# Kernel optimization log

Measured on AMD Instinct MI355X. Metric: run time of the kernel, lower is better.

The kernel has to match this reference:

```python
import jax, jax.numpy as jnp
import numpy as np

DIM = 1024
N_HEADS = 16
HEAD_DIM = DIM // N_HEADS
SCALE = HEAD_DIM ** -0.5


def setup_inputs() -> dict:
    key = jax.random.key(0)
    kx, kq, kk, kv = jax.random.split(key, 4)
    x = jax.random.normal(kx, (2, 2048, DIM), dtype=jnp.float32)
    bv_q = jax.random.normal(kq, (N_HEADS, HEAD_DIM), dtype=jnp.float32) * 0.02
    bv_k = jax.random.normal(kk, (N_HEADS, HEAD_DIM), dtype=jnp.float32) * 0.02
    bv_v = jax.random.normal(kv, (N_HEADS, HEAD_DIM), dtype=jnp.float32) * 0.02
    return {"x": x, "bv_q": bv_q, "bv_k": bv_k, "bv_v": bv_v}


def reference(x, bv_q, bv_k, bv_v):
    B, T, D = x.shape
    H, HD = N_HEADS, HEAD_DIM
    x_h = x.reshape(B, T, H, HD)
    # sign-gated Q/K/V (sign of binding vectors; elementwise +/-1 gating)
    Q = x_h * jnp.sign(bv_q)  # [B,T,H,HD]
    K = x_h * jnp.sign(bv_k)
    V = x_h * jnp.sign(bv_v)
    # causal scores, sigmoid gating (no softmax)
    scores = jnp.einsum('bqhd,bkhd->bhqk', Q, K) * SCALE  # [B,H,T,T]
    causal = jnp.tril(jnp.ones((T, T), dtype=bool))
    attn = jnp.where(causal, jax.nn.sigmoid(scores * 4.0), 0.0)
    out = jnp.einsum('bhqk,bkhd->bqhd', attn, V)  # [B,T,H,HD]
    return out.reshape(B, T, D)
```

## Files before the change

### kernel.cpp

```cpp
#include <hip/hip_runtime.h>
#include <hip/hip_bf16.h>
#include <stdint.h>

#define DIM 1024
#define T_LEN 2048
#define NB 2
#define NH 16
#define HD 64
#define NQT 32

typedef float f32x4 __attribute__((ext_vector_type(4)));
typedef float f32x16 __attribute__((ext_vector_type(16)));
typedef __bf16 bf16x8 __attribute__((ext_vector_type(8)));
typedef __bf16 bf16x2 __attribute__((ext_vector_type(2)));
typedef unsigned int u32;
typedef unsigned int u32x4 __attribute__((ext_vector_type(4)));

__device__ __forceinline__ float sgnf(float v) {
    return (v > 0.f) ? 1.f : ((v < 0.f) ? -1.f : 0.f);
}

__device__ __forceinline__ float sigmoid_half(float v) {
    return __builtin_amdgcn_rcpf(1.f + __builtin_amdgcn_exp2f(-0.72134752f * v));
}

__device__ __forceinline__ u32 pack2(float p0, float p1) {
    bf16x2 t = {(__bf16)p0, (__bf16)p1};
    return __builtin_bit_cast(u32, t);
}

__device__ __forceinline__ void gload16(const __bf16* g, __bf16* l) {
    __builtin_amdgcn_global_load_lds(
        (__attribute__((address_space(1))) void*)g,
        (__attribute__((address_space(3))) void*)l,
        16, 0, 0);
}

__global__ __launch_bounds__(256) void prep_kernel(
    const float* __restrict__ x, __bf16* __restrict__ xb, __bf16* __restrict__ xt)
{
    __shared__ __align__(16) __bf16 tile[64][72];

    const int bid = blockIdx.x;
    const int h = bid & 15, tmp = bid >> 4, tt = tmp & 31, b = tmp >> 5;
    const int tid = threadIdx.x;
    const int r = tid >> 2, c0 = (tid & 3) * 16;

    const size_t rowbase = ((size_t)(b * T_LEN + tt * 64 + r)) * DIM + h * HD + c0;
    const float* xp = x + rowbase;

    __bf16 v[16];
    #pragma unroll
    for (int i = 0; i < 16; i += 4) {
        f32x4 f = *(const f32x4*)(xp + i);
        #pragma unroll
        for (int j = 0; j < 4; ++j) v[i + j] = (__bf16)f[j];
    }
    bf16x8 s0, s1;
    #pragma unroll
    for (int j = 0; j < 8; ++j) { s0[j] = v[j]; s1[j] = v[8 + j]; }
    *(bf16x8*)(xb + rowbase)     = s0;
    *(bf16x8*)(xb + rowbase + 8) = s1;
    *(bf16x8*)&tile[r][c0]     = s0;
    *(bf16x8*)&tile[r][c0 + 8] = s1;

    __syncthreads();

    const int d = tid >> 2, t0c = (tid & 3) * 16;
    __bf16 ov[16];
    #pragma unroll
    for (int i = 0; i < 16; ++i) ov[i] = tile[t0c + i][d];
    bf16x8 o0, o1;
    #pragma unroll
    for (int j = 0; j < 8; ++j) { o0[j] = ov[j]; o1[j] = ov[8 + j]; }
    const size_t obase = ((size_t)((b * NH + h) * HD + d)) * T_LEN + tt * 64 + t0c;
    *(bf16x8*)(xt + obase)     = o0;
    *(bf16x8*)(xt + obase + 8) = o1;
}

__global__ __launch_bounds__(256, 4) void mba_main(
    const __bf16* __restrict__ xb, const __bf16* __restrict__ xt,
    const float* __restrict__ bvq, const float* __restrict__ bvk,
    const float* __restrict__ bvv, float* __restrict__ out)
{
    __shared__ __align__(16) __bf16 Kb[3][64][64];
    __shared__ __align__(16) __bf16 Vb[2][64][64];

    const int bid = blockIdx.x;
    const int u = bid >> 5;
    const int jj = u >> 3, aa = u & 7;
    const int qt = 8 * jj + ((jj & 1) ? (7 - aa) : aa);
    const int bh = bid & 31;
    const int b = bh >> 4, h = bh & 15;
    const int q0 = qt * 64;

    const int tid = threadIdx.x;
    const int w = tid >> 6, l = tid & 63;
    const int c = l & 31, hi = l >> 5;
    const int qh = w & 1, sh = w >> 1;

    const size_t xb_bh = (size_t)b * T_LEN * DIM + h * HD;
    const size_t xt_bh = (size_t)((b * NH + h) * HD) * T_LEN;

    const int rr = l >> 3;
    const int sw = ((l & 7) ^ rr) << 3;

    auto STAGE_K = [&](int buf, int kvt) {
        const int kv0s = kvt * 64;
        #pragma unroll
        for (int pt = 0; pt < 2; ++pt) {
            const int r0 = w * 8 + pt * 32;
            gload16(xb + xb_bh + (size_t)(kv0s + r0 + rr) * DIM + sw, &Kb[buf][r0][0]);
        }
    };
    auto STAGE_V = [&](int buf, int kvt) {
        const int kv0s = kvt * 64;
        #pragma unroll
        for (int pt = 0; pt < 2; ++pt) {
            const int r0 = w * 8 + pt * 32;
            gload16(xt + xt_bh + (size_t)(r0 + rr) * T_LEN + kv0s + sw, &Vb[buf][r0][0]);
        }
    };

    STAGE_K(0, 0);
    STAGE_V(0, 0);
    if (qt >= 1) STAGE_K(1, 1);

    bf16x8 qa[4];
    {
        const float* bq = bvq + h * HD;
        const float* bk = bvk + h * HD;
        const int qrow = q0 + qh * 32 + c;
        #pragma unroll
        for (int m = 0; m < 4; ++m) {
            const int d0 = m * 16 + hi * 8;
            bf16x8 va = *(const bf16x8*)(xb + xb_bh + (size_t)qrow * DIM + d0);
            #pragma unroll
            for (int j = 0; j < 8; ++j) {
                float f = sgnf(bq[d0 + j]) * sgnf(bk[d0 + j]);
                qa[m][j] = (__bf16)((float)va[j] * f);
            }
        }
    }
    float sv[2];
    #pragma unroll
    for (int nd = 0; nd < 2; ++nd) sv[nd] = sgnf(bvv[h * HD + nd * 32 + c]);

    f32x16 o[2];
    #pragma unroll
    for (int nd = 0; nd < 2; ++nd)
        #pragma unroll
        for (int i = 0; i < 16; ++i) o[nd][i] = 0.f;

    int cur = 0;
    const int krow = sh * 32 + c;
    const int swz = (c & 7) << 4;

    for (int t = 0; t <= qt; ++t) {
        const bool last = (t == qt);
        if (last) { asm volatile("s_waitcnt vmcnt(0)" ::: "memory"); }
        else      { asm volatile("s_waitcnt vmcnt(2)" ::: "memory"); }
        __builtin_amdgcn_sched_barrier(0);
        __builtin_amdgcn_s_barrier();
        __builtin_amdgcn_sched_barrier(0);

        if (t + 1 <= qt) STAGE_V((t + 1) & 1, t + 1);
        __builtin_amdgcn_sched_barrier(0);
        if (t + 2 <= qt) {
            int stg = cur + 2; if (stg >= 3) stg -= 3;
            STAGE_K(stg, t + 2);
        }
        __builtin_amdgcn_sched_barrier(0);

        f32x16 ss;
        #pragma unroll
        for (int i = 0; i < 16; ++i) ss[i] = 0.f;
        #pragma unroll
        for (int m = 0; m < 4; ++m) {
            bf16x8 kf = *(const bf16x8*)((const char*)&Kb[cur][krow][0]
                          + ((m * 32 + hi * 16) ^ swz));
            ss = __builtin_amdgcn_mfma_f32_32x32x16_bf16(kf, qa[m], ss, 0, 0, 0);
        }

        u32 W[8];
        #pragma unroll
        for (int i = 0; i < 8; ++i) {
            const int r0 = 2 * i;
            const int sl = (r0 & 3) + 8 * (r0 >> 2) + 4 * hi;
            float p0 = sigmoid_half(ss[r0]);
            float p1 = sigmoid_half(ss[r0 + 1]);
            if (last) {
                const int sg = sh * 32 + sl;
                const int qg = qh * 32 + c;
                if (sg > qg)     p0 = 0.f;
                if (sg + 1 > qg) p1 = 0.f;
            }
            W[i] = pack2(p0, p1);
        }

        asm volatile("v_permlane32_swap_b32 %0, %1" : "+v"(W[0]), "+v"(W[2]));
        asm volatile("v_permlane32_swap_b32 %0, %1" : "+v"(W[1]), "+v"(W[3]));
        asm volatile("v_permlane32_swap_b32 %0, %1" : "+v"(W[4]), "+v"(W[6]));
        asm volatile("v_permlane32_swap_b32 %0, %1" : "+v"(W[5]), "+v"(W[7]));
        bf16x8 pa[2];
        pa[0] = __builtin_bit_cast(bf16x8, (u32x4){W[0], W[1], W[2], W[3]});
        pa[1] = __builtin_bit_cast(bf16x8, (u32x4){W[4], W[5], W[6], W[7]});

        #pragma unroll
        for (int m = 0; m < 2; ++m) {
            #pragma unroll
            for (int nd = 0; nd < 2; ++nd) {
                bf16x8 vf = *(const bf16x8*)((const char*)&Vb[t & 1][nd * 32 + c][0]
                              + ((sh * 64 + m * 32 + hi * 16) ^ swz));
                o[nd] = __builtin_amdgcn_mfma_f32_32x32x16_bf16(pa[m], vf, o[nd], 0, 0, 0);
            }
        }
        cur = (cur == 2) ? 0 : cur + 1;
    }

    __syncthreads();
    float (*osc)[64] = (float(*)[64]) & Kb[0][0][0];

    if (sh == 1) {
        #pragma unroll
        for (int r = 0; r < 16; ++r) {
            const int qloc = (r & 3) + 8 * (r >> 2) + 4 * hi;
            #pragma unroll
            for (int nd = 0; nd < 2; ++nd)
                osc[qh * 32 + qloc][nd * 32 + c] = o[nd][r];
        }
    }
    __syncthreads();
    if (sh == 0) {
        #pragma unroll
        for (int r = 0; r < 16; ++r) {
            const int qloc = (r & 3) + 8 * (r >> 2) + 4 * hi;
            const size_t row = (size_t)(b * T_LEN + q0 + qh * 32 + qloc) * DIM + h * HD;
            #pragma unroll
            for (int nd = 0; nd < 2; ++nd) {
                float val = (o[nd][r] + osc[qh * 32 + qloc][nd * 32 + c]) * sv[nd];
                out[row + nd * 32 + c] = val;
            }
        }
    }
}

__global__ __launch_bounds__(256) void mba_fallback(
    const float* __restrict__ x,
    const float* __restrict__ bvq,
    const float* __restrict__ bvk,
    const float* __restrict__ bvv,
    float* __restrict__ out)
{
    __shared__ __align__(16) __bf16 Kb[64][72];
    __shared__ __align__(16) __bf16 Vt[HD][72];
    __shared__ __align__(16) __bf16 Pb[4][16][72];

    const int bid = blockIdx.x;
    const int qt  = (NQT - 1) - (bid & (NQT - 1));
    const int bh  = bid >> 5;
    const int b   = bh >> 4;
    const int h   = bh & 15;

    const int tid = threadIdx.x;
    const int w   = tid >> 6;
    const int l   = tid & 63;
    const int lq  = l & 15;
    const int lh  = l >> 4;

    const int  q0    = qt * 64;
    const long xbase = ((long)b * T_LEN) * DIM + h * HD;

    bf16x8 qa[2];
    {
        const int   qrow = q0 + w * 16 + lq;
        const float* qp  = x + xbase + (long)qrow * DIM + lh * 8;
        const float* gp  = bvq + h * HD + lh * 8;
        #pragma unroll
        for (int ks = 0; ks < 2; ++ks)
            #pragma unroll
            for (int j = 0; j < 8; ++j)
                qa[ks][j] = (__bf16)(qp[ks * 32 + j] * sgnf(gp[ks * 32 + j]));
    }

    f32x4 o[4];
    #pragma unroll
    for (int n = 0; n < 4; ++n) o[n] = (f32x4){0.f, 0.f, 0.f, 0.f};

    const int r_st = tid >> 2;
    const int c0   = (tid & 3) * 16;
    const float* gk = bvk + h * HD + c0;
    const float* gv = bvv + h * HD + c0;

    for (int kvt = 0; kvt <= qt; ++kvt) {
        const int kv0 = kvt * 64;
        __syncthreads();
        {
            const float* kp = x + xbase + (long)(kv0 + r_st) * DIM + c0;
            __bf16 kb[16];
            #pragma unroll
            for (int i = 0; i < 16; ++i) kb[i] = (__bf16)(kp[i] * sgnf(gk[i]));
            *(bf16x8*)&Kb[r_st][c0]     = *(bf16x8*)&kb[0];
            *(bf16x8*)&Kb[r_st][c0 + 8] = *(bf16x8*)&kb[8];
            #pragma unroll
            for (int i = 0; i < 16; ++i)
                Vt[c0 + i][r_st] = (__bf16)(kp[i] * sgnf(gv[i]));
        }
        __syncthreads();

        f32x4 s[4];
        #pragma unroll
        for (int n = 0; n < 4; ++n) s[n] = (f32x4){0.f, 0.f, 0.f, 0.f};
        #pragma unroll
        for (int ks = 0; ks < 2; ++ks)
            #pragma unroll
            for (int n = 0; n < 4; ++n) {
                bf16x8 kf = *(const bf16x8*)&Kb[n * 16 + lq][ks * 32 + lh * 8];
                s[n] = __builtin_amdgcn_mfma_f32_16x16x32_bf16(qa[ks], kf, s[n], 0, 0, 0);
            }

        const bool diag = (kvt == qt);
        #pragma unroll
        for (int n = 0; n < 4; ++n)
            #pragma unroll
            for (int j = 0; j < 4; ++j) {
                float p = sigmoid_half(s[n][j]);
                if (diag && (n * 16 + lq) > (w * 16 + lh * 4 + j)) p = 0.f;
                Pb[w][lh * 4 + j][n * 16 + lq] = (__bf16)p;
            }

        #pragma unroll
        for (int ks = 0; ks < 2; ++ks) {
            bf16x8 pf = *(const bf16x8*)&Pb[w][lq][ks * 32 + lh * 8];
            #pragma unroll
            for (int n = 0; n < 4; ++n) {
                bf16x8 vf = *(const bf16x8*)&Vt[n * 16 + lq][ks * 32 + lh * 8];
                o[n] = __builtin_amdgcn_mfma_f32_16x16x32_bf16(pf, vf, o[n], 0, 0, 0);
            }
        }
    }

    float* op = out + ((long)b * T_LEN + q0 + w * 16) * DIM + h * HD;
    #pragma unroll
    for (int n = 0; n < 4; ++n)
        #pragma unroll
        for (int j = 0; j < 4; ++j)
            op[(long)(lh * 4 + j) * DIM + n * 16 + lq] = o[n][j];
}

extern "C" void kernel_launch(void* const* d_in, const int* in_sizes, int n_in,
                              void* d_out, int out_size, void* d_ws, size_t ws_size,
                              hipStream_t stream) {
    (void)in_sizes; (void)n_in; (void)out_size;
    const float* x   = (const float*)d_in[0];
    const float* bvq = (const float*)d_in[1];
    const float* bvk = (const float*)d_in[2];
    const float* bvv = (const float*)d_in[3];
    float* out = (float*)d_out;

    const size_t XB_BYTES = (size_t)NB * T_LEN * DIM * sizeof(__bf16);
    const size_t XT_BYTES = XB_BYTES;

    if (ws_size < XB_BYTES + XT_BYTES) {
        mba_fallback<<<NB * NH * NQT, 256, 0, stream>>>(x, bvq, bvk, bvv, out);
        return;
    }

    __bf16* xb = (__bf16*)d_ws;
    __bf16* xt = xb + (size_t)NB * T_LEN * DIM;

    prep_kernel<<<NB * NQT * NH, 256, 0, stream>>>(x, xb, xt);
    mba_main<<<NB * NH * NQT, 256, 0, stream>>>(xb, xt, bvq, bvk, bvv, out);
}
```

Baseline: 47.43 us.

## Fold V sign into prep, switch to double-buffered K/V with priority hints

Moves the sign(bv_v) gating into the transpose prep kernel, so the main kernel no longer multiplies the output by sv at the epilogue. Replaces the 3-stage K ring with 2-stage K/V double buffering that issues both loads one tile ahead and waits on vmcnt(0) every iteration, unrolling the loop by two so buffer indices are constant. Adds s_setprio around the MFMA blocks and a packed-vector form of the sigmoid. The change reduces LDS use but gives K loads less prefetch distance, which may expose more memory latency.

Result: slower. 54.10 us (+14.1%).

```diff
diff --git a/kernel.cpp b/kernel.cpp
--- a/kernel.cpp
+++ b/kernel.cpp
@@ -9,6 +9,7 @@
 #define HD 64
 #define NQT 32
 
+typedef float f32x2 __attribute__((ext_vector_type(2)));
 typedef float f32x4 __attribute__((ext_vector_type(4)));
 typedef float f32x16 __attribute__((ext_vector_type(16)));
 typedef __bf16 bf16x8 __attribute__((ext_vector_type(8)));
@@ -20,10 +21,6 @@
     return (v > 0.f) ? 1.f : ((v < 0.f) ? -1.f : 0.f);
 }
 
-__device__ __forceinline__ float sigmoid_half(float v) {
-    return __builtin_amdgcn_rcpf(1.f + __builtin_amdgcn_exp2f(-0.72134752f * v));
-}
-
 __device__ __forceinline__ u32 pack2(float p0, float p1) {
     bf16x2 t = {(__bf16)p0, (__bf16)p1};
     return __builtin_bit_cast(u32, t);
@@ -37,7 +34,8 @@
 }
 
 __global__ __launch_bounds__(256) void prep_kernel(
-    const float* __restrict__ x, __bf16* __restrict__ xb, __bf16* __restrict__ xt)
+    const float* __restrict__ x, const float* __restrict__ bvv,
+    __bf16* __restrict__ xb, __bf16* __restrict__ xt)
 {
     __shared__ __align__(16) __bf16 tile[64][72];
 
@@ -67,9 +65,10 @@
     __syncthreads();
 
     const int d = tid >> 2, t0c = (tid & 3) * 16;
+    const float g = sgnf(bvv[h * HD + d]);
     __bf16 ov[16];
     #pragma unroll
-    for (int i = 0; i < 16; ++i) ov[i] = tile[t0c + i][d];
+    for (int i = 0; i < 16; ++i) ov[i] = (__bf16)((float)tile[t0c + i][d] * g);
     bf16x8 o0, o1;
     #pragma unroll
     for (int j = 0; j < 8; ++j) { o0[j] = ov[j]; o1[j] = ov[8 + j]; }
@@ -81,9 +80,9 @@
 __global__ __launch_bounds__(256, 4) void mba_main(
     const __bf16* __restrict__ xb, const __bf16* __restrict__ xt,
     const float* __restrict__ bvq, const float* __restrict__ bvk,
-    const float* __restrict__ bvv, float* __restrict__ out)
+    float* __restrict__ out)
 {
-    __shared__ __align__(16) __bf16 Kb[3][64][64];
+    __shared__ __align__(16) __bf16 Kb[2][64][64];
     __shared__ __align__(16) __bf16 Vb[2][64][64];
 
     const int bid = blockIdx.x;
@@ -124,7 +123,6 @@
 
     STAGE_K(0, 0);
     STAGE_V(0, 0);
-    if (qt >= 1) STAGE_K(1, 1);
 
     bf16x8 qa[4];
     {
@@ -142,9 +140,6 @@
             }
         }
     }
-    float sv[2];
-    #pragma unroll
-    for (int nd = 0; nd < 2; ++nd) sv[nd] = sgnf(bvv[h * HD + nd * 32 + c]);
 
     f32x16 o[2];
     #pragma unroll
@@ -152,44 +147,46 @@
         #pragma unroll
         for (int i = 0; i < 16; ++i) o[nd][i] = 0.f;
 
-    int cur = 0;
     const int krow = sh * 32 + c;
     const int swz = (c & 7) << 4;
 
-    for (int t = 0; t <= qt; ++t) {
-        const bool last = (t == qt);
-        if (last) { asm volatile("s_waitcnt vmcnt(0)" ::: "memory"); }
-        else      { asm volatile("s_waitcnt vmcnt(2)" ::: "memory"); }
+    auto bodyfn = [&](int t, int pb) {
+        const bool diag = (t == qt);
+        asm volatile("s_waitcnt vmcnt(0)" ::: "memory");
         __builtin_amdgcn_sched_barrier(0);
         __builtin_amdgcn_s_barrier();
         __builtin_amdgcn_sched_barrier(0);
 
-        if (t + 1 <= qt) STAGE_V((t + 1) & 1, t + 1);
+        if (t + 1 <= qt) {
+            STAGE_V(pb ^ 1, t + 1);
+            STAGE_K(pb ^ 1, t + 1);
+        }
         __builtin_amdgcn_sched_barrier(0);
-        if (t + 2 <= qt) {
-            int stg = cur + 2; if (stg >= 3) stg -= 3;
-            STAGE_K(stg, t + 2);
-        }
-        __builtin_amdgcn_sched_barrier(0);
 
         f32x16 ss;
         #pragma unroll
         for (int i = 0; i < 16; ++i) ss[i] = 0.f;
+        __builtin_amdgcn_s_setprio(1);
         #pragma unroll
         for (int m = 0; m < 4; ++m) {
-            bf16x8 kf = *(const bf16x8*)((const char*)&Kb[cur][krow][0]
+            bf16x8 kf = *(const bf16x8*)((const char*)&Kb[pb][krow][0]
                           + ((m * 32 + hi * 16) ^ swz));
             ss = __builtin_amdgcn_mfma_f32_32x32x16_bf16(kf, qa[m], ss, 0, 0, 0);
         }
+        __builtin_amdgcn_s_setprio(0);
 
         u32 W[8];
         #pragma unroll
         for (int i = 0; i < 8; ++i) {
             const int r0 = 2 * i;
             const int sl = (r0 & 3) + 8 * (r0 >> 2) + 4 * hi;
-            float p0 = sigmoid_half(ss[r0]);
-            float p1 = sigmoid_half(ss[r0 + 1]);
-            if (last) {
+            f32x2 z = {ss[r0], ss[r0 + 1]};
+            z = z * (-0.72134752f);
+            f32x2 e = {__builtin_amdgcn_exp2f(z.x), __builtin_amdgcn_exp2f(z.y)};
+            e = e + 1.0f;
+            float p0 = __builtin_amdgcn_rcpf(e.x);
+            float p1 = __builtin_amdgcn_rcpf(e.y);
+            if (diag) {
                 const int sg = sh * 32 + sl;
                 const int qg = qh * 32 + c;
                 if (sg > qg)     p0 = 0.f;
@@ -206,16 +203,22 @@
         pa[0] = __builtin_bit_cast(bf16x8, (u32x4){W[0], W[1], W[2], W[3]});
         pa[1] = __builtin_bit_cast(bf16x8, (u32x4){W[4], W[5], W[6], W[7]});
 
+        __builtin_amdgcn_s_setprio(1);
         #pragma unroll
         for (int m = 0; m < 2; ++m) {
             #pragma unroll
             for (int nd = 0; nd < 2; ++nd) {
-                bf16x8 vf = *(const bf16x8*)((const char*)&Vb[t & 1][nd * 32 + c][0]
+                bf16x8 vf = *(const bf16x8*)((const char*)&Vb[pb][nd * 32 + c][0]
                               + ((sh * 64 + m * 32 + hi * 16) ^ swz));
                 o[nd] = __builtin_amdgcn_mfma_f32_32x32x16_bf16(pa[m], vf, o[nd], 0, 0, 0);
             }
         }
-        cur = (cur == 2) ? 0 : cur + 1;
+        __builtin_amdgcn_s_setprio(0);
+    };
+
+    for (int t = 0; t <= qt; t += 2) {
+        bodyfn(t, 0);
+        if (t + 1 <= qt) bodyfn(t + 1, 1);
     }
 
     __syncthreads();
@@ -225,9 +228,8 @@
         #pragma unroll
         for (int r = 0; r < 16; ++r) {
             const int qloc = (r & 3) + 8 * (r >> 2) + 4 * hi;
-            #pragma unroll
-            for (int nd = 0; nd < 2; ++nd)
-                osc[qh * 32 + qloc][nd * 32 + c] = o[nd][r];
+            osc[qh * 32 + qloc][c]      = o[0][r];
+            osc[qh * 32 + qloc][32 + c] = o[1][r];
         }
     }
     __syncthreads();
@@ -236,11 +238,8 @@
         for (int r = 0; r < 16; ++r) {
             const int qloc = (r & 3) + 8 * (r >> 2) + 4 * hi;
             const size_t row = (size_t)(b * T_LEN + q0 + qh * 32 + qloc) * DIM + h * HD;
-            #pragma unroll
-            for (int nd = 0; nd < 2; ++nd) {
-                float val = (o[nd][r] + osc[qh * 32 + qloc][nd * 32 + c]) * sv[nd];
-                out[row + nd * 32 + c] = val;
-            }
+            out[row + c]      = o[0][r] + osc[qh * 32 + qloc][c];
+            out[row + 32 + c] = o[1][r] + osc[qh * 32 + qloc][32 + c];
         }
     }
 }
@@ -324,7 +323,9 @@
         for (int n = 0; n < 4; ++n)
             #pragma unroll
             for (int j = 0; j < 4; ++j) {
-                float p = sigmoid_half(s[n][j]);
+                float sc = s[n][j];
+                float p = __builtin_amdgcn_rcpf(
+                              1.f + __builtin_amdgcn_exp2f(-0.72134752f * sc));
                 if (diag && (n * 16 + lq) > (w * 16 + lh * 4 + j)) p = 0.f;
                 Pb[w][lh * 4 + j][n * 16 + lq] = (__bf16)p;
             }
@@ -369,6 +370,6 @@
     __bf16* xb = (__bf16*)d_ws;
     __bf16* xt = xb + (size_t)NB * T_LEN * DIM;
 
-    prep_kernel<<<NB * NQT * NH, 256, 0, stream>>>(x, xb, xt);
-    mba_main<<<NB * NH * NQT, 256, 0, stream>>>(xb, xt, bvq, bvk, bvv, out);
-}
+    prep_kernel<<<NB * NQT * NH, 256, 0, stream>>>(x, bvv, xb, xt);
+    mba_main<<<NB * NH * NQT, 256, 0, stream>>>(xb, xt, bvq, bvk, out);
+}
```
